# Kernel optimization log

Measured on AMD Instinct MI355X. Metric: run time of the kernel, lower is better.

The kernel has to match this reference:

```python
import jax, jax.numpy as jnp
import numpy as np

B, DIM, H, W = 8, 128, 64, 64
K = 7                      # involution kernel size
PAD = (K - 1) // 2
GC = 16                    # group_channels (RedNet involution default)
G = DIM // GC              # groups = 8
RED = 4                    # reduction_ratio
BN_EPS = 1e-5
LN_EPS = 1e-6


def setup_inputs() -> dict:
    key = jax.random.key(0)
    ks = jax.random.split(key, 8)
    s = lambda k, sh: jax.random.normal(k, sh, jnp.float32) * 0.02
    return {
        "x": jax.random.normal(ks[0], (B, DIM, H, W), jnp.float32),
        # involution kernel-generation branch: 1x1 conv -> BN -> ReLU -> 1x1 conv
        "conv1_w": s(ks[1], (DIM // RED, DIM)), "conv1_b": jnp.zeros((DIM // RED,), jnp.float32),
        "bn_g": jnp.ones((DIM // RED,), jnp.float32), "bn_b": jnp.zeros((DIM // RED,), jnp.float32),
        "bn_mean": jnp.zeros((DIM // RED,), jnp.float32), "bn_var": jnp.ones((DIM // RED,), jnp.float32),
        "conv2_w": s(ks[2], (K * K * G, DIM // RED)), "conv2_b": jnp.zeros((K * K * G,), jnp.float32),
        # LayerNorm (channels_last)
        "ln_g": jnp.ones((DIM,), jnp.float32), "ln_b": jnp.zeros((DIM,), jnp.float32),
        # pointwise MLP
        "pw1_w": s(ks[3], (2 * DIM, DIM)), "pw1_b": jnp.zeros((2 * DIM,), jnp.float32),
        "pw2_w": s(ks[4], (DIM, 2 * DIM)), "pw2_b": jnp.zeros((DIM,), jnp.float32),
    }


def _involution(x, conv1_w, conv1_b, bn_g, bn_b, bn_mean, bn_var, conv2_w, conv2_b):
    # kernel-generation: 1x1 conv -> BN(eval) -> ReLU -> 1x1 conv
    t = jnp.einsum('oc,bchw->bohw', conv1_w, x) + conv1_b[None, :, None, None]
    scale = bn_g * jax.lax.rsqrt(bn_var + BN_EPS)
    t = t * scale[None, :, None, None] + (bn_b - bn_mean * scale)[None, :, None, None]
    t = jax.nn.relu(t)
    wgt = jnp.einsum('oc,bchw->bohw', conv2_w, t) + conv2_b[None, :, None, None]
    wgt = wgt.reshape(B, G, K * K, H, W)            # per-pixel kernels
    # apply per-pixel kernel: accumulate over window offsets (no unfold materialization)
    xp = jnp.pad(x, ((0, 0), (0, 0), (PAD, PAD), (PAD, PAD)))
    xg = xp.reshape(B, G, GC, H + 2 * PAD, W + 2 * PAD)
    out = jnp.zeros((B, G, GC, H, W), x.dtype)
    for i in range(K):
        for j in range(K):
            patch = xg[:, :, :, i:i + H, j:j + W]   # [B,G,GC,H,W]
            out = out + wgt[:, :, i * K + j][:, :, None] * patch
    return out.reshape(B, DIM, H, W)


def reference(x, conv1_w, conv1_b, bn_g, bn_b, bn_mean, bn_var, conv2_w, conv2_b,
              ln_g, ln_b, pw1_w, pw1_b, pw2_w, pw2_b):
    identity = x
    y = _involution(x, conv1_w, conv1_b, bn_g, bn_b, bn_mean, bn_var, conv2_w, conv2_b)
    y = y.transpose(0, 2, 3, 1)                     # NCHW -> NHWC
    mu = jnp.mean(y, axis=-1, keepdims=True)
    var = jnp.var(y, axis=-1, keepdims=True)
    y = (y - mu) * jax.lax.rsqrt(var + LN_EPS) * ln_g + ln_b
    y = jnp.einsum('bhwc,fc->bhwf', y, pw1_w) + pw1_b
    y = jax.nn.gelu(y, approximate=False)           # torch nn.GELU default (erf)
    # dropout: inference mode -> identity
    y = jnp.einsum('bhwf,cf->bhwc', y, pw2_w) + pw2_b
    y = y.transpose(0, 3, 1, 2)                     # NHWC -> NCHW
    return y + identity
```

## Files before the change

### kernel.cpp

```cpp
#include <hip/hip_runtime.h>
#include <hip/hip_bf16.h>
#include <math.h>

#define Bn   8
#define DIM  128
#define Hs   64
#define Ws   64
#define GC   16
#define Gn   8
#define CMID 32
#define NW   392
#define NWP  416

typedef __bf16 bf16x8 __attribute__((ext_vector_type(8)));
typedef float  f32x4  __attribute__((ext_vector_type(4)));
typedef _Float16 h2v  __attribute__((ext_vector_type(2)));
typedef __fp16   fp16x2 __attribute__((ext_vector_type(2)));

__device__ __forceinline__ f32x4 mfma16(bf16x8 a, bf16x8 b, f32x4 c) {
    return __builtin_amdgcn_mfma_f32_16x16x32_bf16(a, b, c, 0, 0, 0);
}
__device__ __forceinline__ __bf16 tobf(float v) {
    __hip_bfloat16 h = __float2bfloat16(v);
    return *reinterpret_cast<__bf16*>(&h);
}
__device__ __forceinline__ unsigned su16(float f) {
    __hip_bfloat16 h = __float2bfloat16(f);
    return (unsigned)*reinterpret_cast<unsigned short*>(&h);
}
__device__ __forceinline__ unsigned pk2u(float a, float b) {
    fp16x2 p = __builtin_amdgcn_cvt_pkrtz(a, b);
    return __builtin_bit_cast(unsigned, p);
}
__device__ __forceinline__ h2v u2h(unsigned u) { return __builtin_bit_cast(h2v, u); }
__device__ __forceinline__ float gelu_t(float v) {
    float u = 0.7978845608f * v * fmaf(0.044715f, v * v, 1.0f);
    float t = __builtin_amdgcn_exp2f(fminf(u, 30.f) * 2.885390082f);
    return v * t * __builtin_amdgcn_rcpf(t + 1.0f);
}

__global__ __launch_bounds__(256) void k0_cvt(const float* __restrict__ w1,
        const float* __restrict__ w2,
        const float* __restrict__ pw1, const float* __restrict__ pw2,
        const float* __restrict__ x,
        __hip_bfloat16* __restrict__ w1b, __hip_bfloat16* __restrict__ w2b,
        __hip_bfloat16* __restrict__ mw1b, __hip_bfloat16* __restrict__ mw2b,
        unsigned* __restrict__ xpad) {
    int T = blockIdx.x * 256 + threadIdx.x;
    if (T < 32768) {
        int i = T;
        if (i < CMID * DIM) w1b[i] = __float2bfloat16(w1[i]);
        if (i < NWP * CMID)
            w2b[i] = (i < NW * CMID) ? __float2bfloat16(w2[i]) : __float2bfloat16(0.f);
        {
            int f = i >> 7, j = i & 127;
            int t4 = j >> 5, k = j & 31;
            int g = k >> 2, pi = (k >> 1) & 1, sel = k & 1;
            mw1b[i] = __float2bfloat16(pw1[f * 128 + g * 16 + t4 * 2 + pi + 8 * sel]);
        }
        mw2b[i] = __float2bfloat16(pw2[i]);
    }
#pragma unroll
    for (int e = 0; e < 5; ++e) {
        int idx = T + e * 524288;
        if (idx < 512 * 5040) {
            int c8 = idx / 5040;
            int rem = idx - c8 * 5040;
            int prow = rem / 72, pcol = rem - prow * 72;
            int hh = prow - 3, wc = pcol - 3;
            int bb = c8 >> 6, gg = (c8 >> 3) & 7, cc = c8 & 7;
            unsigned v = 0;
            if ((unsigned)hh < 64u && (unsigned)wc < 64u) {
                size_t src = ((size_t)(bb * DIM + gg * GC + cc)) * 4096 + hh * 64 + wc;
                v = pk2u(x[src], x[src + 8 * 4096]);
            }
            xpad[(size_t)c8 * 5040 + rem] = v;
        }
    }
}

__global__ __launch_bounds__(64) void k_all(const float* __restrict__ x,
        const unsigned* __restrict__ xpad,
        const __hip_bfloat16* __restrict__ w1b, const float* __restrict__ b1v,
        const float* __restrict__ bng, const float* __restrict__ bnb,
        const float* __restrict__ bnm, const float* __restrict__ bnv,
        const __hip_bfloat16* __restrict__ w2b, const float* __restrict__ b2v,
        const float* __restrict__ lng, const float* __restrict__ lnb,
        const __hip_bfloat16* __restrict__ mw1b, const float* __restrict__ mb1,
        const __hip_bfloat16* __restrict__ mw2b, const float* __restrict__ mb2,
        float* __restrict__ out) {
    __shared__ __align__(16) char uni[17216];
    __hip_bfloat16* tsh   = (__hip_bfloat16*)uni;
    h2v*            wgt2T = (h2v*)(uni + 1088);
    __hip_bfloat16* ylds  = (__hip_bfloat16*)(uni + 4416);
    __hip_bfloat16* zsh   = (__hip_bfloat16*)(uni + 8768);

    int bid = blockIdx.x;
    int b = bid & 7;
    int rest = bid >> 3;
    int h = rest >> 2, wq = rest & 3;
    int w0 = wq * 16;
    int lane = threadIdx.x;
    int l15 = lane & 15, l4 = lane >> 4;
    int px = l15, t4 = l4;

    bf16x8 afr[4];
#pragma unroll
    for (int ks = 0; ks < 4; ++ks)
#pragma unroll
        for (int i = 0; i < 8; ++i) {
            int c = ks * 32 + l4 * 8 + i;
            afr[ks][i] = tobf(x[(((size_t)b * DIM + c) * Hs + h) * Ws + w0 + l15]);
        }
    f32x4 acc1[2];
    acc1[0] = (f32x4){0.f, 0.f, 0.f, 0.f};
    acc1[1] = (f32x4){0.f, 0.f, 0.f, 0.f};
#pragma unroll
    for (int nt = 0; nt < 2; ++nt)
#pragma unroll
        for (int ks = 0; ks < 4; ++ks) {
            bf16x8 bf = *(const bf16x8*)&w1b[(nt * 16 + l15) * DIM + ks * 32 + l4 * 8];
            acc1[nt] = mfma16(afr[ks], bf, acc1[nt]);
        }
#pragma unroll
    for (int nt = 0; nt < 2; ++nt) {
        int o = nt * 16 + l15;
        float sc = bng[o] * rsqrtf(bnv[o] + 1e-5f);
        float sh = bnb[o] - bnm[o] * sc;
        float bv = b1v[o];
#pragma unroll
        for (int r = 0; r < 4; ++r) {
            float v = (acc1[nt][r] + bv) * sc + sh;
            tsh[(l4 * 4 + r) * 34 + o] = __float2bfloat16(fmaxf(v, 0.f));
        }
    }
    bf16x8 a_t = *(const bf16x8*)&tsh[l15 * 34 + l4 * 8];

    unsigned ypk[16];
    float s = 0.f, ss = 0.f;

#pragma unroll 1
    for (int g = 0; g < Gn; ++g) {
        unsigned Ax[14], Bx[14];
#pragma unroll
        for (int pi = 0; pi < 2; ++pi)
#pragma unroll
            for (int r = 0; r < 7; ++r) {
                const unsigned* rp = xpad + (size_t)(b * 64 + g * 8 + t4 * 2 + pi) * 5040
                                   + (h + r) * 72 + w0;
                Ax[pi * 7 + r] = rp[px];
                Bx[pi * 7 + r] = rp[px + 16];
            }

        {
            f32x4 ac[4];
#pragma unroll
            for (int nt = 0; nt < 4; ++nt) ac[nt] = (f32x4){0.f, 0.f, 0.f, 0.f};
#pragma unroll
            for (int nt = 0; nt < 4; ++nt) {
                bf16x8 bf = *(const bf16x8*)&w2b[(size_t)(g * 49 + nt * 16 + l15) * CMID + l4 * 8];
                ac[nt] = mfma16(a_t, bf, ac[nt]);
            }
#pragma unroll
            for (int nt = 0; nt < 4; ++nt) {
                int p = nt * 16 + l15;
                if (p < 49) {
                    float bias = b2v[g * 49 + p];
#pragma unroll
                    for (int r = 0; r < 4; ++r) {
                        _Float16 hf16 = (_Float16)(ac[nt][r] + bias);
                        wgt2T[(l4 * 4 + r) * 52 + p] = (h2v){hf16, hf16};
                    }
                }
            }
        }

        h2v wv[52];
#pragma unroll
        for (int u = 0; u < 13; ++u) {
            uint4 t = *(const uint4*)&wgt2T[px * 52 + u * 4];
            wv[u * 4 + 0] = u2h(t.x);
            wv[u * 4 + 1] = u2h(t.y);
            wv[u * 4 + 2] = u2h(t.z);
            wv[u * 4 + 3] = u2h(t.w);
        }

#define INV_TAP(J)                                                                          \
        {                                                                                   \
            unsigned ta = (unsigned)__builtin_amdgcn_update_dpp(                            \
                0, (int)A, 0x100 + J, 0xF, 0xF, false);                                     \
            unsigned tb = (unsigned)__builtin_amdgcn_update_dpp(                            \
                0, (int)B, 0x110 + (16 - J), 0xF, 0xF, false);                              \
            hacc = wv[r * 7 + J] * u2h(ta | tb) + hacc;                                     \
        }
        float acc[2][2];
#pragma unroll
        for (int pi = 0; pi < 2; ++pi) {
            float ax = 0.f, ay2 = 0.f;
#pragma unroll
            for (int r = 0; r < 7; ++r) {
                unsigned A = Ax[pi * 7 + r], B = Bx[pi * 7 + r];
                h2v hacc = wv[r * 7] * u2h(A);
                INV_TAP(1) INV_TAP(2) INV_TAP(3)
                INV_TAP(4) INV_TAP(5) INV_TAP(6)
                ax += (float)hacc.x;
                ay2 += (float)hacc.y;
            }
            acc[pi][0] = ax; acc[pi][1] = ay2;
        }
#undef INV_TAP
#pragma unroll
        for (int pi = 0; pi < 2; ++pi) {
            ypk[g * 2 + pi] = su16(acc[pi][0]) | (su16(acc[pi][1]) << 16);
            s += acc[pi][0] + acc[pi][1];
            ss = fmaf(acc[pi][0], acc[pi][0], fmaf(acc[pi][1], acc[pi][1], ss));
        }
    }

    s += __shfl_xor(s, 16);  s += __shfl_xor(s, 32);
    ss += __shfl_xor(ss, 16); ss += __shfl_xor(ss, 32);
    float mu = s * (1.f / DIM);
    float var = ss * (1.f / DIM) - mu * mu;
    float rs = rsqrtf(var + 1e-6f);

    {
        unsigned wds[16];
#pragma unroll
        for (int g = 0; g < 8; ++g)
#pragma unroll
            for (int pi = 0; pi < 2; ++pi) {
                unsigned wk = ypk[g * 2 + pi];
                float lo = __uint_as_float(wk << 16);
                float hi = __uint_as_float(wk & 0xffff0000u);
                int c0 = g * 16 + t4 * 2 + pi, c1 = c0 + 8;
                lo = (lo - mu) * rs * lng[c0] + lnb[c0];
                hi = (hi - mu) * rs * lng[c1] + lnb[c1];
                wds[g * 2 + pi] = su16(lo) | (su16(hi) << 16);
            }
        __hip_bfloat16* dst = ylds + px * 136 + t4 * 32;
#pragma unroll
        for (int c4 = 0; c4 < 4; ++c4) {
            uint4 vv = {wds[c4 * 4 + 0], wds[c4 * 4 + 1], wds[c4 * 4 + 2], wds[c4 * 4 + 3]};
            *(uint4*)&dst[c4 * 8] = vv;
        }
    }

    bf16x8 ay[4];
#pragma unroll
    for (int ks = 0; ks < 4; ++ks)
        ay[ks] = *(const bf16x8*)&ylds[l15 * 136 + ks * 32 + l4 * 8];

#pragma unroll
    for (int half = 0; half < 2; ++half) {
        f32x4 zac[8];
#pragma unroll
        for (int n = 0; n < 8; ++n) zac[n] = (f32x4){0.f, 0.f, 0.f, 0.f};
#pragma unroll
        for (int ks = 0; ks < 4; ++ks)
#pragma unroll
            for (int n = 0; n < 8; ++n) {
                int nt = half * 8 + n;
                bf16x8 bf = *(const bf16x8*)&mw1b[(nt * 16 + l15) * DIM + ks * 32 + l4 * 8];
                zac[n] = mfma16(ay[ks], bf, zac[n]);
            }
#pragma unroll
        for (int n = 0; n < 8; ++n) {
            int nt = half * 8 + n;
            float bv = mb1[nt * 16 + l15];
#pragma unroll
            for (int r = 0; r < 4; ++r) {
                float v = gelu_t(zac[n][r] + bv);
                zsh[(l4 * 4 + r) * 264 + nt * 16 + l15] = __float2bfloat16(v);
            }
        }
    }

    bf16x8 az[8];
#pragma unroll
    for (int ks = 0; ks < 8; ++ks)
        az[ks] = *(const bf16x8*)&zsh[l15 * 264 + ks * 32 + l4 * 8];

    f32x4 oac[8];
#pragma unroll
    for (int n = 0; n < 8; ++n) oac[n] = (f32x4){0.f, 0.f, 0.f, 0.f};
#pragma unroll
    for (int ks = 0; ks < 8; ++ks)
#pragma unroll
        for (int n = 0; n < 8; ++n) {
            bf16x8 bf = *(const bf16x8*)&mw2b[(n * 16 + l15) * 256 + ks * 32 + l4 * 8];
            oac[n] = mfma16(az[ks], bf, oac[n]);
        }

    float4 xr[8];
#pragma unroll
    for (int n = 0; n < 8; ++n) {
        int c = n * 16 + l15;
        xr[n] = *(const float4*)&x[(((size_t)b * DIM + c) * Hs + h) * Ws + w0 + l4 * 4];
    }
#pragma unroll
    for (int n = 0; n < 8; ++n) {
        int c = n * 16 + l15;
        float bv = mb2[c];
        size_t gi = (((size_t)b * DIM + c) * Hs + h) * Ws + w0 + l4 * 4;
        float4 o;
        o.x = oac[n][0] + bv + xr[n].x;
        o.y = oac[n][1] + bv + xr[n].y;
        o.z = oac[n][2] + bv + xr[n].z;
        o.w = oac[n][3] + bv + xr[n].w;
        *(float4*)&out[gi] = o;
    }
}

extern "C" void kernel_launch(void* const* d_in, const int* in_sizes, int n_in,
                              void* d_out, int out_size, void* d_ws, size_t ws_size,
                              hipStream_t stream) {
    const float* x       = (const float*)d_in[0];
    const float* conv1_w = (const float*)d_in[1];
    const float* conv1_b = (const float*)d_in[2];
    const float* bn_g    = (const float*)d_in[3];
    const float* bn_b    = (const float*)d_in[4];
    const float* bn_mean = (const float*)d_in[5];
    const float* bn_var  = (const float*)d_in[6];
    const float* conv2_w = (const float*)d_in[7];
    const float* conv2_b = (const float*)d_in[8];
    const float* ln_g    = (const float*)d_in[9];
    const float* ln_b    = (const float*)d_in[10];
    const float* pw1_w   = (const float*)d_in[11];
    const float* pw1_b   = (const float*)d_in[12];
    const float* pw2_w   = (const float*)d_in[13];
    const float* pw2_b   = (const float*)d_in[14];
    float* out = (float*)d_out;

    char* ws = (char*)d_ws;
    __hip_bfloat16* w1b  = (__hip_bfloat16*)ws;
    __hip_bfloat16* w2b  = (__hip_bfloat16*)(ws + 8192);
    __hip_bfloat16* mw1b = (__hip_bfloat16*)(ws + 34816);
    __hip_bfloat16* mw2b = (__hip_bfloat16*)(ws + 100352);
    unsigned* xpad       = (unsigned*)(ws + (1 << 20));

    hipLaunchKernelGGL(k0_cvt, dim3(2048), dim3(256), 0, stream,
                       conv1_w, conv2_w, pw1_w, pw2_w, x,
                       w1b, w2b, mw1b, mw2b, xpad);
    hipLaunchKernelGGL(k_all, dim3(Bn * Hs * 4), dim3(64), 0, stream,
                       x, xpad, w1b, conv1_b, bn_g, bn_b, bn_mean, bn_var,
                       w2b, conv2_b, ln_g, ln_b,
                       mw1b, pw1_b, mw2b, pw2_b, out);
}
```

Baseline: 67.17 us.

## Split fused involution+MLP block across two wavefronts per tile

```diff
diff --git a/kernel.cpp b/kernel.cpp
--- a/kernel.cpp
+++ b/kernel.cpp
@@ -54,9 +54,9 @@
             w2b[i] = (i < NW * CMID) ? __float2bfloat16(w2[i]) : __float2bfloat16(0.f);
         {
             int f = i >> 7, j = i & 127;
-            int t4 = j >> 5, k = j & 31;
-            int g = k >> 2, pi = (k >> 1) & 1, sel = k & 1;
-            mw1b[i] = __float2bfloat16(pw1[f * 128 + g * 16 + t4 * 2 + pi + 8 * sel]);
+            int wv_ = j >> 6, t4 = (j >> 4) & 3, gl = (j >> 2) & 3;
+            int pi = (j >> 1) & 1, sel = j & 1;
+            mw1b[i] = __float2bfloat16(pw1[f * 128 + (wv_ * 4 + gl) * 16 + t4 * 2 + pi + 8 * sel]);
         }
         mw2b[i] = __float2bfloat16(pw2[i]);
     }
@@ -79,7 +79,7 @@
     }
 }
 
-__global__ __launch_bounds__(64) void k_all(const float* __restrict__ x,
+__global__ __launch_bounds__(128) void k_all(const float* __restrict__ x,
         const unsigned* __restrict__ xpad,
         const __hip_bfloat16* __restrict__ w1b, const float* __restrict__ b1v,
         const float* __restrict__ bng, const float* __restrict__ bnb,
@@ -89,20 +89,23 @@
         const __hip_bfloat16* __restrict__ mw1b, const float* __restrict__ mb1,
         const __hip_bfloat16* __restrict__ mw2b, const float* __restrict__ mb2,
         float* __restrict__ out) {
-    __shared__ __align__(16) char uni[17216];
+    __shared__ __align__(16) char uni[12800];
+    __shared__ float psA[32], psB[32];
     __hip_bfloat16* tsh   = (__hip_bfloat16*)uni;
     h2v*            wgt2T = (h2v*)(uni + 1088);
-    __hip_bfloat16* ylds  = (__hip_bfloat16*)(uni + 4416);
-    __hip_bfloat16* zsh   = (__hip_bfloat16*)(uni + 8768);
+    __hip_bfloat16* ylds  = (__hip_bfloat16*)uni;
+    __hip_bfloat16* zsh   = (__hip_bfloat16*)(uni + 4352);
 
     int bid = blockIdx.x;
     int b = bid & 7;
     int rest = bid >> 3;
     int h = rest >> 2, wq = rest & 3;
     int w0 = wq * 16;
-    int lane = threadIdx.x;
+    int tid = threadIdx.x, lane = tid & 63, w = tid >> 6;
     int l15 = lane & 15, l4 = lane >> 4;
     int px = l15, t4 = l4;
+
+    h2v* wgw = wgt2T + w * 832;
 
     bf16x8 afr[4];
 #pragma unroll
@@ -112,35 +115,32 @@
             int c = ks * 32 + l4 * 8 + i;
             afr[ks][i] = tobf(x[(((size_t)b * DIM + c) * Hs + h) * Ws + w0 + l15]);
         }
-    f32x4 acc1[2];
-    acc1[0] = (f32x4){0.f, 0.f, 0.f, 0.f};
-    acc1[1] = (f32x4){0.f, 0.f, 0.f, 0.f};
-#pragma unroll
-    for (int nt = 0; nt < 2; ++nt)
+    {
+        f32x4 acc1 = (f32x4){0.f, 0.f, 0.f, 0.f};
 #pragma unroll
         for (int ks = 0; ks < 4; ++ks) {
-            bf16x8 bf = *(const bf16x8*)&w1b[(nt * 16 + l15) * DIM + ks * 32 + l4 * 8];
-            acc1[nt] = mfma16(afr[ks], bf, acc1[nt]);
-        }
-#pragma unroll
-    for (int nt = 0; nt < 2; ++nt) {
-        int o = nt * 16 + l15;
+            bf16x8 bf = *(const bf16x8*)&w1b[(w * 16 + l15) * DIM + ks * 32 + l4 * 8];
+            acc1 = mfma16(afr[ks], bf, acc1);
+        }
+        int o = w * 16 + l15;
         float sc = bng[o] * rsqrtf(bnv[o] + 1e-5f);
         float sh = bnb[o] - bnm[o] * sc;
         float bv = b1v[o];
 #pragma unroll
         for (int r = 0; r < 4; ++r) {
-            float v = (acc1[nt][r] + bv) * sc + sh;
+            float v = (acc1[r] + bv) * sc + sh;
             tsh[(l4 * 4 + r) * 34 + o] = __float2bfloat16(fmaxf(v, 0.f));
         }
     }
+    __syncthreads();
     bf16x8 a_t = *(const bf16x8*)&tsh[l15 * 34 + l4 * 8];
 
-    unsigned ypk[16];
+    unsigned ypk[8];
     float s = 0.f, ss = 0.f;
 
 #pragma unroll 1
-    for (int g = 0; g < Gn; ++g) {
+    for (int gl = 0; gl < 4; ++gl) {
+        int g = w * 4 + gl;
         unsigned Ax[14], Bx[14];
 #pragma unroll
         for (int pi = 0; pi < 2; ++pi)
@@ -169,7 +169,7 @@
 #pragma unroll
                     for (int r = 0; r < 4; ++r) {
                         _Float16 hf16 = (_Float16)(ac[nt][r] + bias);
-                        wgt2T[(l4 * 4 + r) * 52 + p] = (h2v){hf16, hf16};
+                        wgw[(l4 * 4 + r) * 52 + p] = (h2v){hf16, hf16};
                     }
                 }
             }
@@ -178,7 +178,7 @@
         h2v wv[52];
 #pragma unroll
         for (int u = 0; u < 13; ++u) {
-            uint4 t = *(const uint4*)&wgt2T[px * 52 + u * 4];
+            uint4 t = *(const uint4*)&wgw[px * 52 + u * 4];
             wv[u * 4 + 0] = u2h(t.x);
             wv[u * 4 + 1] = u2h(t.y);
             wv[u * 4 + 2] = u2h(t.z);
@@ -211,7 +211,7 @@
 #undef INV_TAP
 #pragma unroll
         for (int pi = 0; pi < 2; ++pi) {
-            ypk[g * 2 + pi] = su16(acc[pi][0]) | (su16(acc[pi][1]) << 16);
+            ypk[gl * 2 + pi] = su16(acc[pi][0]) | (su16(acc[pi][1]) << 16);
             s += acc[pi][0] + acc[pi][1];
             ss = fmaf(acc[pi][0], acc[pi][0], fmaf(acc[pi][1], acc[pi][1], ss));
         }
@@ -219,39 +219,42 @@
 
     s += __shfl_xor(s, 16);  s += __shfl_xor(s, 32);
     ss += __shfl_xor(ss, 16); ss += __shfl_xor(ss, 32);
-    float mu = s * (1.f / DIM);
-    float var = ss * (1.f / DIM) - mu * mu;
+    if (lane < 16) { psA[w * 16 + px] = s; psB[w * 16 + px] = ss; }
+    __syncthreads();
+    float sa = psA[px] + psA[16 + px];
+    float sb = psB[px] + psB[16 + px];
+    float mu = sa * (1.f / DIM);
+    float var = sb * (1.f / DIM) - mu * mu;
     float rs = rsqrtf(var + 1e-6f);
 
     {
-        unsigned wds[16];
-#pragma unroll
-        for (int g = 0; g < 8; ++g)
+        unsigned wds[8];
+#pragma unroll
+        for (int gl = 0; gl < 4; ++gl)
 #pragma unroll
             for (int pi = 0; pi < 2; ++pi) {
-                unsigned wk = ypk[g * 2 + pi];
+                unsigned wk = ypk[gl * 2 + pi];
                 float lo = __uint_as_float(wk << 16);
                 float hi = __uint_as_float(wk & 0xffff0000u);
-                int c0 = g * 16 + t4 * 2 + pi, c1 = c0 + 8;
+                int c0 = (w * 4 + gl) * 16 + t4 * 2 + pi, c1 = c0 + 8;
                 lo = (lo - mu) * rs * lng[c0] + lnb[c0];
                 hi = (hi - mu) * rs * lng[c1] + lnb[c1];
-                wds[g * 2 + pi] = su16(lo) | (su16(hi) << 16);
-            }
-        __hip_bfloat16* dst = ylds + px * 136 + t4 * 32;
-#pragma unroll
-        for (int c4 = 0; c4 < 4; ++c4) {
-            uint4 vv = {wds[c4 * 4 + 0], wds[c4 * 4 + 1], wds[c4 * 4 + 2], wds[c4 * 4 + 3]};
-            *(uint4*)&dst[c4 * 8] = vv;
-        }
-    }
+                wds[gl * 2 + pi] = su16(lo) | (su16(hi) << 16);
+            }
+        __hip_bfloat16* dst = ylds + px * 136 + w * 64 + t4 * 16;
+        uint4 v1 = {wds[0], wds[1], wds[2], wds[3]};
+        uint4 v2 = {wds[4], wds[5], wds[6], wds[7]};
+        *(uint4*)&dst[0] = v1;
+        *(uint4*)&dst[8] = v2;
+    }
+    __syncthreads();
 
     bf16x8 ay[4];
 #pragma unroll
     for (int ks = 0; ks < 4; ++ks)
         ay[ks] = *(const bf16x8*)&ylds[l15 * 136 + ks * 32 + l4 * 8];
 
-#pragma unroll
-    for (int half = 0; half < 2; ++half) {
+    {
         f32x4 zac[8];
 #pragma unroll
         for (int n = 0; n < 8; ++n) zac[n] = (f32x4){0.f, 0.f, 0.f, 0.f};
@@ -259,13 +262,13 @@
         for (int ks = 0; ks < 4; ++ks)
 #pragma unroll
             for (int n = 0; n < 8; ++n) {
-                int nt = half * 8 + n;
+                int nt = w * 8 + n;
                 bf16x8 bf = *(const bf16x8*)&mw1b[(nt * 16 + l15) * DIM + ks * 32 + l4 * 8];
                 zac[n] = mfma16(ay[ks], bf, zac[n]);
             }
 #pragma unroll
         for (int n = 0; n < 8; ++n) {
-            int nt = half * 8 + n;
+            int nt = w * 8 + n;
             float bv = mb1[nt * 16 + l15];
 #pragma unroll
             for (int r = 0; r < 4; ++r) {
@@ -274,32 +277,34 @@
             }
         }
     }
+    __syncthreads();
 
     bf16x8 az[8];
 #pragma unroll
     for (int ks = 0; ks < 8; ++ks)
         az[ks] = *(const bf16x8*)&zsh[l15 * 264 + ks * 32 + l4 * 8];
 
-    f32x4 oac[8];
-#pragma unroll
-    for (int n = 0; n < 8; ++n) oac[n] = (f32x4){0.f, 0.f, 0.f, 0.f};
+    f32x4 oac[4];
+#pragma unroll
+    for (int n = 0; n < 4; ++n) oac[n] = (f32x4){0.f, 0.f, 0.f, 0.f};
 #pragma unroll
     for (int ks = 0; ks < 8; ++ks)
 #pragma unroll
-        for (int n = 0; n < 8; ++n) {
-            bf16x8 bf = *(const bf16x8*)&mw2b[(n * 16 + l15) * 256 + ks * 32 + l4 * 8];
+        for (int n = 0; n < 4; ++n) {
+            int nt = w * 4 + n;
+            bf16x8 bf = *(const bf16x8*)&mw2b[(nt * 16 + l15) * 256 + ks * 32 + l4 * 8];
             oac[n] = mfma16(az[ks], bf, oac[n]);
         }
 
-    float4 xr[8];
-#pragma unroll
-    for (int n = 0; n < 8; ++n) {
-        int c = n * 16 + l15;
+    float4 xr[4];
+#pragma unroll
+    for (int n = 0; n < 4; ++n) {
+        int c = (w * 4 + n) * 16 + l15;
         xr[n] = *(const float4*)&x[(((size_t)b * DIM + c) * Hs + h) * Ws + w0 + l4 * 4];
     }
 #pragma unroll
-    for (int n = 0; n < 8; ++n) {
-        int c = n * 16 + l15;
+    for (int n = 0; n < 4; ++n) {
+        int c = (w * 4 + n) * 16 + l15;
         float bv = mb2[c];
         size_t gi = (((size_t)b * DIM + c) * Hs + h) * Ws + w0 + l4 * 4;
         float4 o;
@@ -341,7 +346,7 @@
     hipLaunchKernelGGL(k0_cvt, dim3(2048), dim3(256), 0, stream,
                        conv1_w, conv2_w, pw1_w, pw2_w, x,
                        w1b, w2b, mw1b, mw2b, xpad);
-    hipLaunchKernelGGL(k_all, dim3(Bn * Hs * 4), dim3(64), 0, stream,
+    hipLaunchKernelGGL(k_all, dim3(Bn * Hs * 4), dim3(128), 0, stream,
                        x, xpad, w1b, conv1_b, bn_g, bn_b, bn_mean, bn_var,
                        w2b, conv2_b, ln_g, ln_b,
                        mw1b, pw1_b, mw2b, pw2_b, out);
```

New measurement: 76.90 us. 14.5% more time.
